# Kernel optimization log

Measured on AMD Instinct MI355X. Metric: run time of the kernel, lower is better.

The kernel has to match this reference:

```python
import jax, jax.numpy as jnp
import numpy as np
import math

B, S, H = 2, 2048, 2048
NH, HD = 16, 64  # head_dim = H // (2*NH)
LAMBDA_INIT = 0.5


def setup_inputs() -> dict:
    key = jax.random.key(0)
    ks = jax.random.split(key, 6)
    std = 1.0 / math.sqrt(H)
    hidden_states = jax.random.normal(ks[0], (B, S, H), dtype=jnp.float32)
    # Linear weights stored as [in, out] (x @ W)
    Wq = jax.random.normal(ks[1], (H, 2 * NH * HD), dtype=jnp.float32) * std
    Wk = jax.random.normal(ks[2], (H, 2 * NH * HD), dtype=jnp.float32) * std
    Wv = jax.random.normal(ks[3], (H, NH * HD), dtype=jnp.float32) * std
    Wo = jax.random.normal(ks[4], (NH * HD, H), dtype=jnp.float32) * (1.0 / math.sqrt(NH * HD))
    lambda_param = jnp.log(jnp.asarray(1.0 / math.tanh(LAMBDA_INIT), dtype=jnp.float32))
    # causal additive mask, (B, 1, S, S)
    causal = jnp.tril(jnp.ones((S, S), dtype=bool))
    attention_mask = jnp.where(causal, 0.0, jnp.finfo(jnp.float32).min)[None, None]
    attention_mask = jnp.broadcast_to(attention_mask, (B, 1, S, S))
    return {"hidden_states": hidden_states, "attention_mask": attention_mask,
            "Wq": Wq, "Wk": Wk, "Wv": Wv, "Wo": Wo, "lambda_param": lambda_param}


def reference(hidden_states, attention_mask, Wq, Wk, Wv, Wo, lambda_param):
    bsz, q_len, _ = hidden_states.shape
    scaling = HD ** -0.5

    q_all = (hidden_states @ Wq).reshape(bsz, q_len, 2 * NH, HD).transpose(0, 2, 1, 3)
    k_all = (hidden_states @ Wk).reshape(bsz, q_len, 2 * NH, HD).transpose(0, 2, 1, 3)
    v = (hidden_states @ Wv).reshape(bsz, q_len, NH, HD).transpose(0, 2, 1, 3)
    q1, q2 = q_all[:, :NH], q_all[:, NH:]
    k1, k2 = k_all[:, :NH], k_all[:, NH:]

    lam = jnp.tanh(jax.nn.softplus(lambda_param))
    scores1 = jnp.einsum('bhqd,bhkd->bhqk', q1, k1) * scaling
    scores2 = jnp.einsum('bhqd,bhkd->bhqk', q2, k2) * scaling
    attn_scores = scores1 - lam * scores2 + attention_mask
    attn_weights = jax.nn.softmax(attn_scores.astype(jnp.float32), axis=-1).astype(q1.dtype)

    attn_out = jnp.einsum('bhqk,bhkd->bhqd', attn_weights, v)
    attn_out = attn_out.transpose(0, 2, 1, 3).reshape(bsz, q_len, NH * HD)
    return attn_out @ Wo
```

## Files before the change

### kernel.cpp

```cpp
#include <hip/hip_runtime.h>
#include <hip/hip_bf16.h>

#define B_ 2
#define S_ 2048
#define H_ 2048
#define NH_ 16
#define HD_ 64
#define DQ_ 2048
#define DV_ 1024
#define QKS_ 4096

using bf16x8 = __attribute__((ext_vector_type(8))) __bf16;
using f32x4  = __attribute__((ext_vector_type(4))) float;

typedef __attribute__((address_space(1))) unsigned int u32g;
typedef __attribute__((address_space(3))) unsigned int u32l;

__device__ __forceinline__ void gload_lds16(const __bf16* g, __bf16* l) {
  __builtin_amdgcn_global_load_lds((u32g*)g, (u32l*)l, 16, 0, 0);
}

__device__ __forceinline__ int swz(int row, int colb, int strideB) {
  return row * strideB + (colb ^ (((row ^ (row >> 3)) & 7) << 4));
}
__device__ __forceinline__ int fxor(int row) { return (row ^ (row >> 3)) & 7; }
__device__ __forceinline__ int fxor4(int row) { return (row ^ (row >> 2)) & 3; }


__global__ __launch_bounds__(256) void cast_hidden(const float* __restrict__ in,
                                                   __bf16* __restrict__ out, int n) {
  int i = (blockIdx.x * 256 + threadIdx.x) * 8;
  if (i >= n) return;
  float4 a = *reinterpret_cast<const float4*>(in + i);
  float4 b = *reinterpret_cast<const float4*>(in + i + 4);
  bf16x8 o;
  o[0] = (__bf16)a.x; o[1] = (__bf16)a.y; o[2] = (__bf16)a.z; o[3] = (__bf16)a.w;
  o[4] = (__bf16)b.x; o[5] = (__bf16)b.y; o[6] = (__bf16)b.z; o[7] = (__bf16)b.w;
  *reinterpret_cast<bf16x8*>(out + i) = o;
}

__global__ __launch_bounds__(256) void transpose_cast(const float* __restrict__ in,
                                                      __bf16* __restrict__ out, int R, int C) {
  __shared__ float tile[32][33];
  int tx = threadIdx.x & 31, ty = threadIdx.x >> 5;
  int c0 = blockIdx.x * 32, r0 = blockIdx.y * 32;
  for (int i = 0; i < 32; i += 8)
    tile[ty + i][tx] = in[(size_t)(r0 + ty + i) * C + c0 + tx];
  __syncthreads();
  for (int i = 0; i < 32; i += 8)
    out[(size_t)(c0 + ty + i) * R + r0 + tx] = (__bf16)tile[tx][ty + i];
}


template <typename OutT>
__global__ __launch_bounds__(256) void gemm_bt(const __bf16* __restrict__ A,
                                               const __bf16* __restrict__ Bt,
                                               OutT* __restrict__ C,
                                               int M, int N, int K) {
  __shared__ __bf16 As[2][128 * 32];
  __shared__ __bf16 Bs[2][128 * 32];
  const int nx = gridDim.x;
  int id = blockIdx.y * nx + blockIdx.x;
  const int cpx = (nx * gridDim.y) >> 3;
  id = (id & 7) * cpx + (id >> 3);
  const int bm = id / nx, bn = id % nx;

  const int tid = threadIdx.x;
  const int wid = tid >> 6, lane = tid & 63;
  const int wm = wid >> 1, wn = wid & 1;
  const int g = lane >> 4, c = lane & 15;

  f32x4 acc[4][4] = {};
  const __bf16* Abase = A + (size_t)(bm * 128) * K;
  const __bf16* Bbase = Bt + (size_t)(bn * 128) * K;
  const int srow = wid * 16 + (lane >> 2);
  const int scol = (lane & 3) * 8;
  const int nk = K >> 5;

  auto stage = [&](int p, int kt) {
    int k0 = kt * 32;
    gload_lds16(Abase + (size_t)srow * K + k0 + scol,        &As[p][(wid * 16) * 32]);
    gload_lds16(Abase + (size_t)(srow + 64) * K + k0 + scol, &As[p][(64 + wid * 16) * 32]);
    gload_lds16(Bbase + (size_t)srow * K + k0 + scol,        &Bs[p][(wid * 16) * 32]);
    gload_lds16(Bbase + (size_t)(srow + 64) * K + k0 + scol, &Bs[p][(64 + wid * 16) * 32]);
  };

  stage(0, 0);
  stage(1, 1);

  for (int kt = 0; kt < nk; ++kt) {
    const int p = kt & 1;
    if (kt + 1 < nk) {
      asm volatile("s_waitcnt vmcnt(4)" ::: "memory");
    } else {
      asm volatile("s_waitcnt vmcnt(0)" ::: "memory");
    }
    __builtin_amdgcn_s_barrier();
    __builtin_amdgcn_sched_barrier(0);

    bf16x8 af[4], bfv[4];
#pragma unroll
    for (int i = 0; i < 4; ++i)
      af[i] = *reinterpret_cast<const bf16x8*>(&As[p][(wm * 64 + i * 16 + c) * 32 + g * 8]);
#pragma unroll
    for (int i = 0; i < 4; ++i)
      bfv[i] = *reinterpret_cast<const bf16x8*>(&Bs[p][(wn * 64 + i * 16 + c) * 32 + g * 8]);
#pragma unroll
    for (int m = 0; m < 4; ++m)
#pragma unroll
      for (int n = 0; n < 4; ++n)
        acc[m][n] = __builtin_amdgcn_mfma_f32_16x16x32_bf16(af[m], bfv[n], acc[m][n], 0, 0, 0);

    __builtin_amdgcn_sched_barrier(0);
    __builtin_amdgcn_s_barrier();
    if (kt + 2 < nk) stage(p, kt + 2);
  }

#pragma unroll
  for (int m = 0; m < 4; ++m)
#pragma unroll
    for (int n = 0; n < 4; ++n)
#pragma unroll
      for (int r = 0; r < 4; ++r) {
        int row = bm * 128 + wm * 64 + m * 16 + g * 4 + r;
        int col = bn * 128 + wn * 64 + n * 16 + c;
        float v = acc[m][n][r];
        if constexpr (sizeof(OutT) == 2)
          C[(size_t)row * N + col] = (OutT)(__bf16)v;
        else
          C[(size_t)row * N + col] = v;
      }
}


template <typename OutT>
__global__ __launch_bounds__(512, 2) void gemm256(const __bf16* __restrict__ A,
                                                  const __bf16* __restrict__ Bt,
                                                  OutT* __restrict__ C,
                                                  int M, int N, int K) {
  __shared__ __bf16 As[2][256 * 64];
  __shared__ __bf16 Bs[2][256 * 64];
  const int nx = gridDim.x;
  int id = blockIdx.y * nx + blockIdx.x;
  const int cpx = (nx * gridDim.y) >> 3;
  id = (id & 7) * cpx + (id >> 3);
  const int bm = id / nx, bn = id % nx;

  const int tid = threadIdx.x;
  const int wid = tid >> 6, lane = tid & 63;
  const int wm = wid >> 2, wn = wid & 3;
  const int g = lane >> 4, c = lane & 15;

  f32x4 acc[8][4] = {};
  bf16x8 af[4][2];
  bf16x8 bfv[4][2];
  const __bf16* Abase = A + (size_t)(bm * 256) * K;
  const __bf16* Bbase = Bt + (size_t)(bn * 256) * K;
  const int niter = K >> 7;

  auto stageA = [&](int p, int half, int kt) {
#pragma unroll
    for (int j = 0; j < 2; ++j) {
      int row = half * 128 + j * 64 + wid * 8 + (lane >> 3);
      int gc = (lane & 7) ^ (row & 7);
      gload_lds16(Abase + (size_t)row * K + kt * 64 + gc * 8,
                  &As[p][(half * 128 + j * 64 + wid * 8) * 64]);
    }
  };
  auto stageB = [&](int p, int half, int kt) {
#pragma unroll
    for (int j = 0; j < 2; ++j) {
      int row = half * 128 + j * 64 + wid * 8 + (lane >> 3);
      int gc = (lane & 7) ^ (row & 7);
      gload_lds16(Bbase + (size_t)row * K + kt * 64 + gc * 8,
                  &Bs[p][(half * 128 + j * 64 + wid * 8) * 64]);
    }
  };
  auto readA = [&](int p, int m, int kk) -> bf16x8 {
    int row = wm * 128 + m * 16 + c;
    int ch = (kk * 4 + g) ^ (row & 7);
    return *reinterpret_cast<const bf16x8*>(&As[p][row * 64 + ch * 8]);
  };
  auto readB = [&](int p, int n, int kk) -> bf16x8 {
    int row = wn * 64 + n * 16 + c;
    int ch = (kk * 4 + g) ^ (row & 7);
    return *reinterpret_cast<const bf16x8*>(&Bs[p][row * 64 + ch * 8]);
  };
  auto quad = [&](int mb, int nb) {
    __builtin_amdgcn_s_setprio(1);
#pragma unroll
    for (int mi = 0; mi < 4; ++mi)
#pragma unroll
      for (int ni = 0; ni < 2; ++ni)
#pragma unroll
        for (int kk = 0; kk < 2; ++kk)
          acc[mb + mi][nb + ni] = __builtin_amdgcn_mfma_f32_16x16x32_bf16(
              af[mi][kk], bfv[nb + ni][kk], acc[mb + mi][nb + ni], 0, 0, 0);
    __builtin_amdgcn_s_setprio(0);
  };
#define BAR1_LGKM()  __builtin_amdgcn_s_barrier(); \
    asm volatile("s_waitcnt lgkmcnt(0)" ::: "memory"); \
    __builtin_amdgcn_sched_barrier(0)
#define BAR2()  __builtin_amdgcn_sched_barrier(0); __builtin_amdgcn_s_barrier()

  stageA(0, 0, 0); stageA(0, 1, 0);
  stageB(0, 0, 0); stageB(0, 1, 0);
  stageB(1, 0, 1); stageB(1, 1, 1);
  asm volatile("s_waitcnt vmcnt(0)" ::: "memory");
  __builtin_amdgcn_s_barrier();

  for (int i = 0; i < niter; ++i) {
    const int t1 = 2 * i + 1;
    const bool more = (i + 1 < niter);
#pragma unroll
    for (int mi = 0; mi < 4; ++mi) { af[mi][0] = readA(0, mi, 0); af[mi][1] = readA(0, mi, 1); }
#pragma unroll
    for (int ni = 0; ni < 2; ++ni) { bfv[ni][0] = readB(0, ni, 0); bfv[ni][1] = readB(0, ni, 1); }
    stageA(1, 0, t1);
    BAR1_LGKM(); quad(0, 0); BAR2();
#pragma unroll
    for (int ni = 2; ni < 4; ++ni) { bfv[ni][0] = readB(0, ni, 0); bfv[ni][1] = readB(0, ni, 1); }
    stageA(1, 1, t1);
    BAR1_LGKM(); quad(0, 2); BAR2();
#pragma unroll
    for (int mi = 0; mi < 4; ++mi) { af[mi][0] = readA(0, 4 + mi, 0); af[mi][1] = readA(0, 4 + mi, 1); }
    if (more) stageB(0, 0, t1 + 1);
    BAR1_LGKM(); quad(4, 0); BAR2();
    if (more) {
      stageB(0, 1, t1 + 1);
      asm volatile("s_waitcnt vmcnt(4)" ::: "memory");
    } else {
      asm volatile("s_waitcnt vmcnt(0)" ::: "memory");
    }
    __builtin_amdgcn_s_barrier();
    __builtin_amdgcn_sched_barrier(0);
    quad(4, 2); BAR2();
#pragma unroll
    for (int mi = 0; mi < 4; ++mi) { af[mi][0] = readA(1, mi, 0); af[mi][1] = readA(1, mi, 1); }
#pragma unroll
    for (int ni = 0; ni < 2; ++ni) { bfv[ni][0] = readB(1, ni, 0); bfv[ni][1] = readB(1, ni, 1); }
    if (more) stageA(0, 0, t1 + 1);
    BAR1_LGKM(); quad(0, 0); BAR2();
#pragma unroll
    for (int ni = 2; ni < 4; ++ni) { bfv[ni][0] = readB(1, ni, 0); bfv[ni][1] = readB(1, ni, 1); }
    if (more) stageA(0, 1, t1 + 1);
    BAR1_LGKM(); quad(0, 2); BAR2();
#pragma unroll
    for (int mi = 0; mi < 4; ++mi) { af[mi][0] = readA(1, 4 + mi, 0); af[mi][1] = readA(1, 4 + mi, 1); }
    if (more) stageB(1, 0, t1 + 2);
    BAR1_LGKM(); quad(4, 0); BAR2();
    if (more) {
      stageB(1, 1, t1 + 2);
      asm volatile("s_waitcnt vmcnt(4)" ::: "memory");
    } else {
      asm volatile("s_waitcnt vmcnt(0)" ::: "memory");
    }
    __builtin_amdgcn_s_barrier();
    __builtin_amdgcn_sched_barrier(0);
    quad(4, 2); BAR2();
  }
#undef BAR1_LGKM
#undef BAR2

#pragma unroll
  for (int m = 0; m < 8; ++m)
#pragma unroll
    for (int n = 0; n < 4; ++n)
#pragma unroll
      for (int r = 0; r < 4; ++r) {
        int row = bm * 256 + wm * 128 + m * 16 + g * 4 + r;
        int col = bn * 256 + wn * 64 + n * 16 + c;
        float v = acc[m][n][r];
        if constexpr (sizeof(OutT) == 2)
          C[(size_t)row * N + col] = (OutT)(__bf16)v;
        else
          C[(size_t)row * N + col] = v;
      }
}


__global__ __launch_bounds__(256, 2) void diffattn(const __bf16* __restrict__ QK,
                                                   const __bf16* __restrict__ V,
                                                   __bf16* __restrict__ OpA,
                                                   __bf16* __restrict__ OpB,
                                                   float* __restrict__ ml,
                                                   const float* __restrict__ lambda_param) {
  __shared__ __bf16 Ks[2][64 * 128];
  __shared__ __bf16 Vs[2][64 * 64];
  __shared__ __bf16 Ps[128 * 64];

  const int y = blockIdx.y;
  const int qt = ((y >> 4) & 1) ? blockIdx.x : (gridDim.x - 1 - blockIdx.x);
  const int bh = y >> 1;
  const int half = y & 1;
  const int b = bh >> 4, h = bh & 15;
  const int tid = threadIdx.x;
  const int w = tid >> 6, lane = tid & 63;
  const int g = lane >> 4, c = lane & 15;
  const float NEG_INF = -__builtin_inff();

  const float lam = tanhf(log1pf(__expf(lambda_param[0])));
  const float L2E = 1.4426950408889634f;
  const float sc1 = 0.125f * L2E;
  const float sc2 = -lam * 0.125f * L2E;

  bf16x8 qf[2][4];
#pragma unroll
  for (int fr = 0; fr < 2; ++fr) {
    int qrow = qt * 128 + w * 32 + fr * 16 + c;
    const __bf16* qbase = QK + (size_t)(b * S_ + qrow) * QKS_;
#pragma unroll
    for (int kk = 0; kk < 4; ++kk) {
      int d = kk * 32 + g * 8;
      const __bf16* src = (d < 64) ? (qbase + h * 64 + d)
                                   : (qbase + DV_ + h * 64 + (d - 64));
      float s = (d < 64) ? sc1 : sc2;
      bf16x8 raw = *reinterpret_cast<const bf16x8*>(src);
      bf16x8 ov;
#pragma unroll
      for (int i = 0; i < 8; ++i) ov[i] = (__bf16)((float)raw[i] * s);
      qf[fr][kk] = ov;
    }
  }

  f32x4 acc[2][4] = {};
  float mrow[2][4], lrow[2][4];
#pragma unroll
  for (int fr = 0; fr < 2; ++fr)
#pragma unroll
    for (int r = 0; r < 4; ++r) { mrow[fr][r] = -1e30f; lrow[fr][r] = 0.f; }

  const int kt0 = half ? (qt + 1) : 0;
  const int kt1 = half ? (2 * qt + 2) : (qt + 1);

  auto stageK = [&](int p, int kt) {
#pragma unroll
    for (int j = 0; j < 4; ++j) {
      int row = w * 16 + j * 4 + (lane >> 4);
      int gc = (lane & 15) ^ fxor(row);
      int s = kt * 64 + row;
      const __bf16* kbase = QK + (size_t)(b * S_ + s) * QKS_ + 2048;
      const __bf16* src = (gc < 8) ? (kbase + h * 64 + gc * 8)
                                   : (kbase + DV_ + h * 64 + (gc - 8) * 8);
      gload_lds16(src, &Ks[p][(w * 16 + j * 4) * 128]);
    }
  };
  auto loadV = [&](int kt, bf16x8* vv) {
#pragma unroll
    for (int j = 0; j < 2; ++j) {
      int flat = tid + j * 256;
      int kv = flat >> 3;
      int d = (flat & 7) * 8;
      vv[j] = *reinterpret_cast<const bf16x8*>(
          V + (size_t)(b * S_ + kt * 64 + kv) * DV_ + h * 64 + d);
    }
  };
  auto scatterV = [&](int p, const bf16x8* vv) {
    char* VsB = (char*)Vs[p];
#pragma unroll
    for (int j = 0; j < 2; ++j) {
      int flat = tid + j * 256;
      int kv = flat >> 3;
      int d = (flat & 7) * 8;
#pragma unroll
      for (int i = 0; i < 8; ++i)
        *reinterpret_cast<__bf16*>(VsB + swz(d + i, kv * 2, 128)) = vv[j][i];
    }
  };

  {
    stageK(0, kt0);
    bf16x8 vv[2];
    loadV(kt0, vv);
    scatterV(0, vv);
    __syncthreads();
  }

  for (int kt = kt0; kt < kt1; ++kt) {
    const int p = (kt - kt0) & 1;
    const bool pre = (kt + 1 < kt1);
    bf16x8 vv[2];
    if (pre) {
      stageK(p ^ 1, kt + 1);
      loadV(kt + 1, vv);
    }

    f32x4 sc[2][4] = {};
    char* KsB = (char*)Ks[p];
    __builtin_amdgcn_s_setprio(1);
#pragma unroll
    for (int f = 0; f < 4; ++f)
#pragma unroll
      for (int kk = 0; kk < 4; ++kk) {
        bf16x8 kf = *reinterpret_cast<const bf16x8*>(
            KsB + swz(f * 16 + c, (kk * 32 + g * 8) * 2, 256));
        sc[0][f] = __builtin_amdgcn_mfma_f32_16x16x32_bf16(qf[0][kk], kf, sc[0][f], 0, 0, 0);
        sc[1][f] = __builtin_amdgcn_mfma_f32_16x16x32_bf16(qf[1][kk], kf, sc[1][f], 0, 0, 0);
      }
    __builtin_amdgcn_s_setprio(0);

    const int dz = kt - 2 * qt;
#pragma unroll
    for (int fr = 0; fr < 2; ++fr) {
      const int wrow0 = w * 32 + fr * 16;
      float pmax[4] = {NEG_INF, NEG_INF, NEG_INF, NEG_INF};
      if (dz >= 0) {
#pragma unroll
        for (int f = 0; f < 4; ++f)
#pragma unroll
          for (int r = 0; r < 4; ++r) {
            float s = sc[fr][f][r];
            if (dz * 64 + f * 16 + c > wrow0 + g * 4 + r) s = NEG_INF;
            sc[fr][f][r] = s;
            pmax[r] = fmaxf(pmax[r], s);
          }
      } else {
#pragma unroll
        for (int f = 0; f < 4; ++f)
#pragma unroll
          for (int r = 0; r < 4; ++r)
            pmax[r] = fmaxf(pmax[r], sc[fr][f][r]);
      }
#pragma unroll
      for (int m = 1; m < 16; m <<= 1)
#pragma unroll
        for (int r = 0; r < 4; ++r)
          pmax[r] = fmaxf(pmax[r], __shfl_xor(pmax[r], m, 64));

      float dm = NEG_INF;
#pragma unroll
      for (int r = 0; r < 4; ++r) dm = fmaxf(dm, pmax[r] - mrow[fr][r]);
      if (!__all(dm <= 8.0f)) {
        float pscl[4];
#pragma unroll
        for (int r = 0; r < 4; ++r) {
          float mnew = fmaxf(mrow[fr][r], pmax[r]);
          pscl[r] = __builtin_amdgcn_exp2f(mrow[fr][r] - mnew);
          mrow[fr][r] = mnew;
        }
#pragma unroll
        for (int r = 0; r < 4; ++r) lrow[fr][r] *= pscl[r];
#pragma unroll
        for (int n = 0; n < 4; ++n)
#pragma unroll
          for (int r = 0; r < 4; ++r)
            acc[fr][n][r] *= pscl[r];
      }

      float rowsum[4] = {0.f, 0.f, 0.f, 0.f};
#pragma unroll
      for (int f = 0; f < 4; ++f)
#pragma unroll
        for (int r = 0; r < 4; ++r) {
          float pv = __builtin_amdgcn_exp2f(sc[fr][f][r] - mrow[fr][r]);
          sc[fr][f][r] = pv;
          rowsum[r] += pv;
        }
#pragma unroll
      for (int m = 1; m < 16; m <<= 1)
#pragma unroll
        for (int r = 0; r < 4; ++r)
          rowsum[r] += __shfl_xor(rowsum[r], m, 64);
#pragma unroll
      for (int r = 0; r < 4; ++r)
        lrow[fr][r] += rowsum[r];

      char* PsB = (char*)Ps;
#pragma unroll
      for (int f = 0; f < 4; ++f)
#pragma unroll
        for (int r = 0; r < 4; ++r)
          *reinterpret_cast<__bf16*>(
              PsB + swz(wrow0 + g * 4 + r, (f * 16 + c) * 2, 128)) = (__bf16)sc[fr][f][r];
    }

    {
      char* PsB = (char*)Ps;
      char* VsB = (char*)Vs[p];
      __builtin_amdgcn_s_setprio(1);
#pragma unroll
      for (int fr = 0; fr < 2; ++fr)
#pragma unroll
        for (int kc = 0; kc < 2; ++kc) {
          bf16x8 pf = *reinterpret_cast<const bf16x8*>(
              PsB + swz(w * 32 + fr * 16 + c, (kc * 32 + g * 8) * 2, 128));
#pragma unroll
          for (int n = 0; n < 4; ++n) {
            bf16x8 vf = *reinterpret_cast<const bf16x8*>(
                VsB + swz(n * 16 + c, (kc * 32 + g * 8) * 2, 128));
            acc[fr][n] = __builtin_amdgcn_mfma_f32_16x16x32_bf16(pf, vf, acc[fr][n], 0, 0, 0);
          }
        }
      __builtin_amdgcn_s_setprio(0);
    }

    if (pre) scatterV(p ^ 1, vv);
    __syncthreads();
  }

  __bf16* Op = half ? OpB : OpA;
#pragma unroll
  for (int fr = 0; fr < 2; ++fr)
#pragma unroll
    for (int n = 0; n < 4; ++n)
#pragma unroll
      for (int r = 0; r < 4; ++r) {
        int q = qt * 128 + w * 32 + fr * 16 + g * 4 + r;
        Op[(size_t)(b * S_ + q) * DV_ + h * 64 + n * 16 + c] = (__bf16)acc[fr][n][r];
      }
  if (c == 0) {
#pragma unroll
    for (int fr = 0; fr < 2; ++fr)
#pragma unroll
      for (int r = 0; r < 4; ++r) {
        int q = qt * 128 + w * 32 + fr * 16 + g * 4 + r;
        float2 v;
        v.x = mrow[fr][r];
        v.y = lrow[fr][r];
        *reinterpret_cast<float2*>(&ml[((size_t)(half * 32 + bh) * S_ + q) * 2]) = v;
      }
  }
}


__global__ __launch_bounds__(256) void merge_halves(const __bf16* __restrict__ OpA,
                                                    const __bf16* __restrict__ OpB,
                                                    const float* __restrict__ ml,
                                                    __bf16* __restrict__ AO) {
  int flat = blockIdx.x * 256 + threadIdx.x;
  int d0 = (flat & 7) * 8;
  int row = flat >> 3;
  int bh = row >> 11, q = row & 2047;
  int b = bh >> 4, h = bh & 15;
  size_t obase = (size_t)(b * S_ + q) * DV_ + h * 64 + d0;

  float2 a2 = *reinterpret_cast<const float2*>(&ml[((size_t)bh * S_ + q) * 2]);
  float2 b2 = *reinterpret_cast<const float2*>(&ml[((size_t)(32 + bh) * S_ + q) * 2]);
  float m = fmaxf(a2.x, b2.x);
  float wA = __builtin_amdgcn_exp2f(a2.x - m);
  float wB = __builtin_amdgcn_exp2f(b2.x - m);
  float inv = 1.0f / (a2.y * wA + b2.y * wB);
  wA *= inv; wB *= inv;

  bf16x8 oa = *reinterpret_cast<const bf16x8*>(OpA + obase);
  bf16x8 ob = *reinterpret_cast<const bf16x8*>(OpB + obase);
  bf16x8 o;
#pragma unroll
  for (int i = 0; i < 8; ++i)
    o[i] = (__bf16)((float)oa[i] * wA + (float)ob[i] * wB);
  *reinterpret_cast<bf16x8*>(AO + obase) = o;
}


extern "C" void kernel_launch(void* const* d_in, const int* in_sizes, int n_in,
                              void* d_out, int out_size, void* d_ws, size_t ws_size,
                              hipStream_t stream) {
  const float* hidden = (const float*)d_in[0];
  const float* Wq = (const float*)d_in[2];
  const float* Wk = (const float*)d_in[3];
  const float* Wv = (const float*)d_in[4];
  const float* Wo = (const float*)d_in[5];
  const float* lambda_param = (const float*)d_in[6];
  float* out = (float*)d_out;

  char* ws = (char*)d_ws;
  size_t off = 0;
  auto alloc = [&](size_t bytes) {
    void* p = ws + off;
    off += (bytes + 255) & ~(size_t)255;
    return p;
  };
  const int M = B_ * S_;
  __bf16* hidb = (__bf16*)alloc((size_t)M * H_ * 2);
  __bf16* TB   = (__bf16*)alloc((size_t)QKS_ * H_ * 2);
  __bf16* QKa  = (__bf16*)alloc((size_t)M * QKS_ * 2);
  __bf16* Va   = (__bf16*)((char*)TB + 4u * 1024 * 1024);
  float*  mlb  = (float*)((char*)TB + 12u * 1024 * 1024);
  __bf16* OpA  = hidb;
  __bf16* OpB  = hidb + (size_t)M * DV_;
  __bf16* AO   = hidb;
  (void)ws_size; (void)in_sizes; (void)n_in; (void)out_size;

  int nh = M * H_;
  cast_hidden<<<nh / (256 * 8), 256, 0, stream>>>(hidden, hidb, nh);

  transpose_cast<<<dim3(DQ_ / 32, H_ / 32), 256, 0, stream>>>(Wq, TB, H_, DQ_);
  transpose_cast<<<dim3(DQ_ / 32, H_ / 32), 256, 0, stream>>>(Wk, TB + (size_t)DQ_ * H_, H_, DQ_);
  gemm256<__bf16><<<dim3(QKS_ / 256, M / 256), 512, 0, stream>>>(hidb, TB, QKa, M, QKS_, H_);

  transpose_cast<<<dim3(DV_ / 32, H_ / 32), 256, 0, stream>>>(Wv, TB, H_, DV_);
  gemm_bt<__bf16><<<dim3(DV_ / 128, M / 128), 256, 0, stream>>>(hidb, TB, Va, M, DV_, H_);

  diffattn<<<dim3(S_ / 128, B_ * NH_ * 2), 256, 0, stream>>>(QKa, Va, OpA, OpB, mlb, lambda_param);
  merge_halves<<<(B_ * NH_ * S_ * HD_ / 8) / 256, 256, 0, stream>>>(OpA, OpB, mlb, AO);

  transpose_cast<<<dim3(H_ / 32, DV_ / 32), 256, 0, stream>>>(Wo, TB, DV_, H_);
  gemm_bt<float><<<dim3(H_ / 128, M / 128), 256, 0, stream>>>(AO, TB, out, M, H_, DV_);
}
```

Measured before the change: 256.2 us.

## Split attention tile over 8 waves with 16 query rows per wave

The diffattn block grows from 256 to 512 threads, so each of 8 waves handles 16 query rows instead of 32, halving per-wave accumulators and score registers. K/V staging is redistributed across the larger block. The row-max shuffle reduction now runs only when the rescale branch is taken. This trades per-wave MFMA reuse of K/V fragments for more waves in flight and lower register pressure. There is a correctness risk: the skipped reduction leaves the all-lanes threshold test using per-lane partial maxima.

```diff
diff --git a/kernel.cpp b/kernel.cpp
--- a/kernel.cpp
+++ b/kernel.cpp
@@ -24,7 +24,6 @@
   return row * strideB + (colb ^ (((row ^ (row >> 3)) & 7) << 4));
 }
 __device__ __forceinline__ int fxor(int row) { return (row ^ (row >> 3)) & 7; }
-__device__ __forceinline__ int fxor4(int row) { return (row ^ (row >> 2)) & 3; }
 
 
 __global__ __launch_bounds__(256) void cast_hidden(const float* __restrict__ in,
@@ -279,7 +278,7 @@
 }
 
 
-__global__ __launch_bounds__(256, 2) void diffattn(const __bf16* __restrict__ QK,
+__global__ __launch_bounds__(512, 4) void diffattn(const __bf16* __restrict__ QK,
                                                    const __bf16* __restrict__ V,
                                                    __bf16* __restrict__ OpA,
                                                    __bf16* __restrict__ OpB,
@@ -304,10 +303,9 @@
   const float sc1 = 0.125f * L2E;
   const float sc2 = -lam * 0.125f * L2E;
 
-  bf16x8 qf[2][4];
-#pragma unroll
-  for (int fr = 0; fr < 2; ++fr) {
-    int qrow = qt * 128 + w * 32 + fr * 16 + c;
+  bf16x8 qf[4];
+  {
+    int qrow = qt * 128 + w * 16 + c;
     const __bf16* qbase = QK + (size_t)(b * S_ + qrow) * QKS_;
 #pragma unroll
     for (int kk = 0; kk < 4; ++kk) {
@@ -319,58 +317,48 @@
       bf16x8 ov;
 #pragma unroll
       for (int i = 0; i < 8; ++i) ov[i] = (__bf16)((float)raw[i] * s);
-      qf[fr][kk] = ov;
+      qf[kk] = ov;
     }
   }
 
-  f32x4 acc[2][4] = {};
-  float mrow[2][4], lrow[2][4];
-#pragma unroll
-  for (int fr = 0; fr < 2; ++fr)
-#pragma unroll
-    for (int r = 0; r < 4; ++r) { mrow[fr][r] = -1e30f; lrow[fr][r] = 0.f; }
+  f32x4 acc[4] = {};
+  float mrow[4], lrow[4];
+#pragma unroll
+  for (int r = 0; r < 4; ++r) { mrow[r] = -1e30f; lrow[r] = 0.f; }
 
   const int kt0 = half ? (qt + 1) : 0;
   const int kt1 = half ? (2 * qt + 2) : (qt + 1);
 
   auto stageK = [&](int p, int kt) {
 #pragma unroll
-    for (int j = 0; j < 4; ++j) {
-      int row = w * 16 + j * 4 + (lane >> 4);
+    for (int j = 0; j < 2; ++j) {
+      int row = w * 8 + j * 4 + (lane >> 4);
       int gc = (lane & 15) ^ fxor(row);
       int s = kt * 64 + row;
       const __bf16* kbase = QK + (size_t)(b * S_ + s) * QKS_ + 2048;
       const __bf16* src = (gc < 8) ? (kbase + h * 64 + gc * 8)
                                    : (kbase + DV_ + h * 64 + (gc - 8) * 8);
-      gload_lds16(src, &Ks[p][(w * 16 + j * 4) * 128]);
+      gload_lds16(src, &Ks[p][(w * 8 + j * 4) * 128]);
     }
   };
   auto loadV = [&](int kt, bf16x8* vv) {
-#pragma unroll
-    for (int j = 0; j < 2; ++j) {
-      int flat = tid + j * 256;
-      int kv = flat >> 3;
-      int d = (flat & 7) * 8;
-      vv[j] = *reinterpret_cast<const bf16x8*>(
-          V + (size_t)(b * S_ + kt * 64 + kv) * DV_ + h * 64 + d);
-    }
+    int kv = tid >> 3;
+    int d = (tid & 7) * 8;
+    vv[0] = *reinterpret_cast<const bf16x8*>(
+        V + (size_t)(b * S_ + kt * 64 + kv) * DV_ + h * 64 + d);
   };
   auto scatterV = [&](int p, const bf16x8* vv) {
     char* VsB = (char*)Vs[p];
-#pragma unroll
-    for (int j = 0; j < 2; ++j) {
-      int flat = tid + j * 256;
-      int kv = flat >> 3;
-      int d = (flat & 7) * 8;
-#pragma unroll
-      for (int i = 0; i < 8; ++i)
-        *reinterpret_cast<__bf16*>(VsB + swz(d + i, kv * 2, 128)) = vv[j][i];
-    }
+    int kv = tid >> 3;
+    int d = (tid & 7) * 8;
+#pragma unroll
+    for (int i = 0; i < 8; ++i)
+      *reinterpret_cast<__bf16*>(VsB + swz(d + i, kv * 2, 128)) = vv[0][i];
   };
 
   {
     stageK(0, kt0);
-    bf16x8 vv[2];
+    bf16x8 vv[1];
     loadV(kt0, vv);
     scatterV(0, vv);
     __syncthreads();
@@ -379,13 +367,13 @@
   for (int kt = kt0; kt < kt1; ++kt) {
     const int p = (kt - kt0) & 1;
     const bool pre = (kt + 1 < kt1);
-    bf16x8 vv[2];
+    bf16x8 vv[1];
     if (pre) {
       stageK(p ^ 1, kt + 1);
       loadV(kt + 1, vv);
     }
 
-    f32x4 sc[2][4] = {};
+    f32x4 sc[4] = {};
     char* KsB = (char*)Ks[p];
     __builtin_amdgcn_s_setprio(1);
 #pragma unroll
@@ -394,84 +382,82 @@
       for (int kk = 0; kk < 4; ++kk) {
         bf16x8 kf = *reinterpret_cast<const bf16x8*>(
             KsB + swz(f * 16 + c, (kk * 32 + g * 8) * 2, 256));
-        sc[0][f] = __builtin_amdgcn_mfma_f32_16x16x32_bf16(qf[0][kk], kf, sc[0][f], 0, 0, 0);
-        sc[1][f] = __builtin_amdgcn_mfma_f32_16x16x32_bf16(qf[1][kk], kf, sc[1][f], 0, 0, 0);
+        sc[f] = __builtin_amdgcn_mfma_f32_16x16x32_bf16(qf[kk], kf, sc[f], 0, 0, 0);
       }
     __builtin_amdgcn_s_setprio(0);
 
     const int dz = kt - 2 * qt;
-#pragma unroll
-    for (int fr = 0; fr < 2; ++fr) {
-      const int wrow0 = w * 32 + fr * 16;
-      float pmax[4] = {NEG_INF, NEG_INF, NEG_INF, NEG_INF};
-      if (dz >= 0) {
-#pragma unroll
-        for (int f = 0; f < 4; ++f)
-#pragma unroll
-          for (int r = 0; r < 4; ++r) {
-            float s = sc[fr][f][r];
-            if (dz * 64 + f * 16 + c > wrow0 + g * 4 + r) s = NEG_INF;
-            sc[fr][f][r] = s;
-            pmax[r] = fmaxf(pmax[r], s);
-          }
-      } else {
-#pragma unroll
-        for (int f = 0; f < 4; ++f)
-#pragma unroll
-          for (int r = 0; r < 4; ++r)
-            pmax[r] = fmaxf(pmax[r], sc[fr][f][r]);
-      }
+    const int wrow0 = w * 16;
+    float pmax[4] = {NEG_INF, NEG_INF, NEG_INF, NEG_INF};
+    if (dz >= 0) {
+#pragma unroll
+      for (int f = 0; f < 4; ++f)
+#pragma unroll
+        for (int r = 0; r < 4; ++r) {
+          float s = sc[f][r];
+          if (dz * 64 + f * 16 + c > wrow0 + g * 4 + r) s = NEG_INF;
+          sc[f][r] = s;
+          pmax[r] = fmaxf(pmax[r], s);
+        }
+    } else {
+#pragma unroll
+      for (int f = 0; f < 4; ++f)
+#pragma unroll
+        for (int r = 0; r < 4; ++r)
+          pmax[r] = fmaxf(pmax[r], sc[f][r]);
+    }
+
+    float dm = NEG_INF;
+#pragma unroll
+    for (int r = 0; r < 4; ++r) dm = fmaxf(dm, pmax[r] - mrow[r]);
+    if (!__all(dm <= 8.0f)) {
 #pragma unroll
       for (int m = 1; m < 16; m <<= 1)
 #pragma unroll
         for (int r = 0; r < 4; ++r)
           pmax[r] = fmaxf(pmax[r], __shfl_xor(pmax[r], m, 64));
-
-      float dm = NEG_INF;
-#pragma unroll
-      for (int r = 0; r < 4; ++r) dm = fmaxf(dm, pmax[r] - mrow[fr][r]);
-      if (!__all(dm <= 8.0f)) {
-        float pscl[4];
-#pragma unroll
-        for (int r = 0; r < 4; ++r) {
-          float mnew = fmaxf(mrow[fr][r], pmax[r]);
-          pscl[r] = __builtin_amdgcn_exp2f(mrow[fr][r] - mnew);
-          mrow[fr][r] = mnew;
-        }
-#pragma unroll
-        for (int r = 0; r < 4; ++r) lrow[fr][r] *= pscl[r];
-#pragma unroll
-        for (int n = 0; n < 4; ++n)
-#pragma unroll
-          for (int r = 0; r < 4; ++r)
-            acc[fr][n][r] *= pscl[r];
+      float pscl[4];
+#pragma unroll
+      for (int r = 0; r < 4; ++r) {
+        float mnew = fmaxf(mrow[r], pmax[r]);
+        pscl[r] = __builtin_amdgcn_exp2f(mrow[r] - mnew);
+        mrow[r] = mnew;
       }
-
-      float rowsum[4] = {0.f, 0.f, 0.f, 0.f};
-#pragma unroll
-      for (int f = 0; f < 4; ++f)
-#pragma unroll
-        for (int r = 0; r < 4; ++r) {
-          float pv = __builtin_amdgcn_exp2f(sc[fr][f][r] - mrow[fr][r]);
-          sc[fr][f][r] = pv;
-          rowsum[r] += pv;
-        }
-#pragma unroll
-      for (int m = 1; m < 16; m <<= 1)
+#pragma unroll
+      for (int r = 0; r < 4; ++r) lrow[r] *= pscl[r];
+#pragma unroll
+      for (int n = 0; n < 4; ++n)
 #pragma unroll
         for (int r = 0; r < 4; ++r)
-          rowsum[r] += __shfl_xor(rowsum[r], m, 64);
+          acc[n][r] *= pscl[r];
+    }
+
+    float rowsum[4] = {0.f, 0.f, 0.f, 0.f};
+#pragma unroll
+    for (int f = 0; f < 4; ++f)
+#pragma unroll
+      for (int r = 0; r < 4; ++r) {
+        float pv = __builtin_amdgcn_exp2f(sc[f][r] - mrow[r]);
+        sc[f][r] = pv;
+        rowsum[r] += pv;
+      }
+#pragma unroll
+    for (int m = 1; m < 16; m <<= 1)
 #pragma unroll
       for (int r = 0; r < 4; ++r)
-        lrow[fr][r] += rowsum[r];
-
+        rowsum[r] += __shfl_xor(rowsum[r], m, 64);
+#pragma unroll
+    for (int r = 0; r < 4; ++r)
+      lrow[r] += rowsum[r];
+
+    {
       char* PsB = (char*)Ps;
 #pragma unroll
       for (int f = 0; f < 4; ++f)
 #pragma unroll
         for (int r = 0; r < 4; ++r)
           *reinterpret_cast<__bf16*>(
-              PsB + swz(wrow0 + g * 4 + r, (f * 16 + c) * 2, 128)) = (__bf16)sc[fr][f][r];
+              PsB + swz(wrow0 + g * 4 + r, (f * 16 + c) * 2, 128)) = (__bf16)sc[f][r];
     }
 
     {
@@ -479,18 +465,16 @@
       char* VsB = (char*)Vs[p];
       __builtin_amdgcn_s_setprio(1);
 #pragma unroll
-      for (int fr = 0; fr < 2; ++fr)
-#pragma unroll
-        for (int kc = 0; kc < 2; ++kc) {
-          bf16x8 pf = *reinterpret_cast<const bf16x8*>(
-              PsB + swz(w * 32 + fr * 16 + c, (kc * 32 + g * 8) * 2, 128));
-#pragma unroll
-          for (int n = 0; n < 4; ++n) {
-            bf16x8 vf = *reinterpret_cast<const bf16x8*>(
-                VsB + swz(n * 16 + c, (kc * 32 + g * 8) * 2, 128));
-            acc[fr][n] = __builtin_amdgcn_mfma_f32_16x16x32_bf16(pf, vf, acc[fr][n], 0, 0, 0);
-          }
+      for (int kc = 0; kc < 2; ++kc) {
+        bf16x8 pf = *reinterpret_cast<const bf16x8*>(
+            PsB + swz(wrow0 + c, (kc * 32 + g * 8) * 2, 128));
+#pragma unroll
+        for (int n = 0; n < 4; ++n) {
+          bf16x8 vf = *reinterpret_cast<const bf16x8*>(
+              VsB + swz(n * 16 + c, (kc * 32 + g * 8) * 2, 128));
+          acc[n] = __builtin_amdgcn_mfma_f32_16x16x32_bf16(pf, vf, acc[n], 0, 0, 0);
         }
+      }
       __builtin_amdgcn_s_setprio(0);
     }
 
@@ -500,25 +484,21 @@
 
   __bf16* Op = half ? OpB : OpA;
 #pragma unroll
-  for (int fr = 0; fr < 2; ++fr)
-#pragma unroll
-    for (int n = 0; n < 4; ++n)
-#pragma unroll
-      for (int r = 0; r < 4; ++r) {
-        int q = qt * 128 + w * 32 + fr * 16 + g * 4 + r;
-        Op[(size_t)(b * S_ + q) * DV_ + h * 64 + n * 16 + c] = (__bf16)acc[fr][n][r];
-      }
+  for (int n = 0; n < 4; ++n)
+#pragma unroll
+    for (int r = 0; r < 4; ++r) {
+      int q = qt * 128 + w * 16 + g * 4 + r;
+      Op[(size_t)(b * S_ + q) * DV_ + h * 64 + n * 16 + c] = (__bf16)acc[n][r];
+    }
   if (c == 0) {
 #pragma unroll
-    for (int fr = 0; fr < 2; ++fr)
-#pragma unroll
-      for (int r = 0; r < 4; ++r) {
-        int q = qt * 128 + w * 32 + fr * 16 + g * 4 + r;
-        float2 v;
-        v.x = mrow[fr][r];
-        v.y = lrow[fr][r];
-        *reinterpret_cast<float2*>(&ml[((size_t)(half * 32 + bh) * S_ + q) * 2]) = v;
-      }
+    for (int r = 0; r < 4; ++r) {
+      int q = qt * 128 + w * 16 + g * 4 + r;
+      float2 v;
+      v.x = mrow[r];
+      v.y = lrow[r];
+      *reinterpret_cast<float2*>(&ml[((size_t)(half * 32 + bh) * S_ + q) * 2]) = v;
+    }
   }
 }
 
@@ -591,7 +571,7 @@
   transpose_cast<<<dim3(DV_ / 32, H_ / 32), 256, 0, stream>>>(Wv, TB, H_, DV_);
   gemm_bt<__bf16><<<dim3(DV_ / 128, M / 128), 256, 0, stream>>>(hidb, TB, Va, M, DV_, H_);
 
-  diffattn<<<dim3(S_ / 128, B_ * NH_ * 2), 256, 0, stream>>>(QKa, Va, OpA, OpB, mlb, lambda_param);
+  diffattn<<<dim3(S_ / 128, B_ * NH_ * 2), 512, 0, stream>>>(QKa, Va, OpA, OpB, mlb, lambda_param);
   merge_halves<<<(B_ * NH_ * S_ * HD_ / 8) / 256, 256, 0, stream>>>(OpA, OpB, mlb, AO);
 
   transpose_cast<<<dim3(H_ / 32, DV_ / 32), 256, 0, stream>>>(Wo, TB, DV_, H_);
```

New measurement: 264.5 us. 1.03x slower.
